# Kernel optimization log

Measured on AMD Instinct MI355X. Metric: run time of the kernel, lower is better.

## Reference

```python
import jax, jax.numpy as jnp
from jax import lax
import numpy as np

BN_EPS = 1e-5
LEAKY_SLOPE = 0.1


def _conv(x, w, stride=1):
    # x: [B,Cin,H,W], w: [Cout,Cin,kh,kw], 'same' padding (padding = k//2)
    p = w.shape[2] // 2
    return lax.conv_general_dilated(x, w, (stride, stride), [(p, p), (p, p)],
                                    dimension_numbers=('NCHW', 'OIHW', 'NCHW'))


def _bn(x, g, b, m, v):
    scale = g / jnp.sqrt(v + BN_EPS)
    return x * scale[None, :, None, None] + (b - m * scale)[None, :, None, None]


def _leaky(x):
    return jnp.where(x >= 0, x, LEAKY_SLOPE * x)


def _identity_grid(s, dtype=jnp.float32):
    # F.affine_grid identity, align_corners=True: grid[i,j] = (x_j, y_i), coords in [-1,1]
    xs = jnp.linspace(-1.0, 1.0, s, dtype=dtype)
    gx, gy = jnp.meshgrid(xs, xs)  # gx[i,j]=xs[j], gy[i,j]=xs[i]
    return jnp.stack([gx, gy], axis=-1)[None]  # [1,s,s,2]


def _grid_sample(img, grid):
    # torch.nn.functional.grid_sample, bilinear, align_corners=True, padding_mode='zeros'
    # img: [B,C,H,W], grid: [B,h,w,2] with grid[...,0]=x(width), grid[...,1]=y(height)
    B, C, H, W = img.shape
    x = (grid[..., 0] + 1.0) * 0.5 * (W - 1)
    y = (grid[..., 1] + 1.0) * 0.5 * (H - 1)
    x0f = jnp.floor(x)
    y0f = jnp.floor(y)
    x0 = x0f.astype(jnp.int32)
    y0 = y0f.astype(jnp.int32)
    x1 = x0 + 1
    y1 = y0 + 1
    wx1 = x - x0f
    wx0 = 1.0 - wx1
    wy1 = y - y0f
    wy0 = 1.0 - wy1

    def corner(xi, yi, w):
        m = ((xi >= 0) & (xi < W) & (yi >= 0) & (yi < H)).astype(img.dtype)
        xc = jnp.clip(xi, 0, W - 1)
        yc = jnp.clip(yi, 0, H - 1)
        gath = jax.vmap(lambda im, yy, xx: im[:, yy, xx])(img, yc, xc)  # [B,C,h,w]
        return gath * (w * m)[:, None]

    return (corner(x0, y0, wx0 * wy0) + corner(x1, y0, wx1 * wy0) +
            corner(x0, y1, wx0 * wy1) + corner(x1, y1, wx1 * wy1))


def _correlation(tgt_list, src_list):
    # corr[b, t, h, w] = sum_c tgt[b,c,t] * src[b,c,(h,w)], concat over feature layers (dim 1)
    outs = []
    for t, s in zip(tgt_list, src_list):
        B, C, H, W = t.shape
        c = jnp.einsum('bct,bcs->bts', t.reshape(B, C, H * W), s.reshape(B, C, H * W))
        outs.append(c.reshape(B, H * W, H, W))
    return jnp.concatenate(outs, axis=1)


def _stn_block(corr, i, w0, bn0_g, bn0_b, bn0_m, bn0_v, w1, bn1_g, bn1_b, bn1_m, bn1_v,
               w2, bn2_g, bn2_b, bn2_m, bn2_v, w3, b3):
    # downscale_factor == 1 (output_size == input_size), upsample-to-same-size is identity
    x = _leaky(_bn(_conv(corr, w0[i], stride=1), bn0_g[i], bn0_b[i], bn0_m[i], bn0_v[i]))
    x = _leaky(_bn(_conv(x, w1[i]), bn1_g[i], bn1_b[i], bn1_m[i], bn1_v[i]))
    x = _leaky(_bn(_conv(x, w2[i]), bn2_g[i], bn2_b[i], bn2_m[i], bn2_v[i]))
    x = _conv(x, w3[i]) + b3[i][None, :, None, None]
    return x  # [B,2,S,S]


def setup_inputs() -> dict:
    key = jax.random.key(0)
    ks = iter(jax.random.split(key, 16))
    B, C, S, L, NS = 8, 256, 32, 2, 3  # batch, feat channels, spatial, n feature layers, n scales
    HW = S * S
    d = {
        'src_layer2': jax.random.normal(next(ks), (B, C, S, S), jnp.float32) * 0.1,
        'src_layer3': jax.random.normal(next(ks), (B, C, S, S), jnp.float32) * 0.1,
        'tgt_layer2': jax.random.normal(next(ks), (B, C, S, S), jnp.float32) * 0.1,
        'tgt_layer3': jax.random.normal(next(ks), (B, C, S, S), jnp.float32) * 0.1,
        'w0': jax.random.normal(next(ks), (NS, HW, HW * L, 1, 1), jnp.float32) * 0.02,
        'w1': jax.random.normal(next(ks), (NS, HW // 2, HW, 3, 3), jnp.float32) * 0.02,
        'w2': jax.random.normal(next(ks), (NS, HW // 4, HW // 2, 3, 3), jnp.float32) * 0.02,
        'w3': jax.random.normal(next(ks), (NS, 2, HW // 4, 1, 1), jnp.float32) * 0.02,
        'b3': jnp.zeros((NS, 2), jnp.float32),
    }
    for j, ch in [(0, HW), (1, HW // 2), (2, HW // 4)]:
        d[f'bn{j}_g'] = jnp.ones((NS, ch), jnp.float32)
        d[f'bn{j}_b'] = jnp.zeros((NS, ch), jnp.float32)
        d[f'bn{j}_m'] = jnp.zeros((NS, ch), jnp.float32)
        d[f'bn{j}_v'] = jnp.ones((NS, ch), jnp.float32)
    return d


def reference(src_layer2, src_layer3, tgt_layer2, tgt_layer3,
              w0, bn0_g, bn0_b, bn0_m, bn0_v,
              w1, bn1_g, bn1_b, bn1_m, bn1_v,
              w2, bn2_g, bn2_b, bn2_m, bn2_v,
              w3, b3):
    src = [src_layer2, src_layer3]
    tgt = [tgt_layer2, tgt_layer3]
    S = src_layer2.shape[-1]
    ident = _identity_grid(S, src_layer2.dtype)  # [1,S,S,2]
    params = (w0, bn0_g, bn0_b, bn0_m, bn0_v, w1, bn1_g, bn1_b, bn1_m, bn1_v,
              w2, bn2_g, bn2_b, bn2_m, bn2_v, w3, b3)

    corr = _correlation(tgt, src)
    flow = jnp.transpose(_stn_block(corr, 0, *params), (0, 2, 3, 1)) + ident  # [B,S,S,2]
    n_scales = w0.shape[0]
    for i in range(1, n_scales):
        warped = [_grid_sample(s, flow) for s in src]
        corr = _correlation(tgt, warped)
        flow = flow + jnp.transpose(_stn_block(corr, i, *params), (0, 2, 3, 1))
    return flow
```

## Files before the change

### kernel.cpp

```cpp
#include <hip/hip_runtime.h>
#include <cstdint>
#include <cstddef>


typedef unsigned short u16;
using bf16x8 = __attribute__((ext_vector_type(8))) short;
using f32x4  = __attribute__((ext_vector_type(4))) float;

constexpr float BN_EPS = 1e-5f;
constexpr float SLOPE  = 0.1f;

__device__ __forceinline__ u16 f2bf(float f) {
    union { float f; uint32_t u; } c; c.f = f;
    uint32_t u = c.u;
    return (u16)((u + 0x7fffu + ((u >> 16) & 1u)) >> 16);
}
__device__ __forceinline__ float bf2f(u16 h) {
    union { uint32_t u; float f; } c; c.u = ((uint32_t)h) << 16;
    return c.f;
}

#define MFMA16(a, b, c) __builtin_amdgcn_mfma_f32_16x16x32_bf16(a, b, c, 0, 0, 0)

constexpr size_t OFF_TGT2B  = 0;
constexpr size_t OFF_TGT3B  = 2097152;
constexpr size_t OFF_SRCT2  = 4194304;
constexpr size_t OFF_SRCT3  = 6291456;
constexpr size_t OFF_WARPT2 = 8388608;
constexpr size_t OFF_WARPT3 = 10485760;
constexpr size_t OFF_W0B    = 12582912;
constexpr size_t OFF_WPK1   = 14680064;
constexpr size_t OFF_WPK2   = 19398656;
constexpr size_t OFF_E      = 20578304;
constexpr size_t OFF_X0T    = 24772608;
constexpr size_t OFF_FLOW   = 33161216;

__global__ __launch_bounds__(256) void cvt_kernel(
    const float* __restrict__ in, u16* __restrict__ out, int n)
{
    int i = (blockIdx.x * 256 + threadIdx.x) * 4;
    if (i + 3 < n) {
        float4 v = *(const float4*)(in + i);
        ushort4 o;
        o.x = f2bf(v.x); o.y = f2bf(v.y); o.z = f2bf(v.z); o.w = f2bf(v.w);
        *(ushort4*)(out + i) = o;
    }
}

__global__ __launch_bounds__(256) void transpose_cvt(
    const float* __restrict__ in, u16* __restrict__ out)
{
    __shared__ float tile[32][33];
    const int s0 = blockIdx.x * 32;
    const int c0 = blockIdx.y * 32;
    const int b  = blockIdx.z;
    const int tid = threadIdx.x;
    const int tx = tid & 31, ty = tid >> 5;
    const float* ib = in + ((size_t)b * 256 + c0) * 1024 + s0;
    #pragma unroll
    for (int r = 0; r < 4; ++r)
        tile[ty + r * 8][tx] = ib[(size_t)(ty + r * 8) * 1024 + tx];
    __syncthreads();
    u16* ob = out + ((size_t)b * 1024 + s0) * 256 + c0;
    #pragma unroll
    for (int r = 0; r < 4; ++r) {
        int s = ty + r * 8;
        ob[(size_t)s * 256 + tx] = f2bf(tile[tx][s]);
    }
}

__global__ __launch_bounds__(256) void pack_conv_w(
    const float* __restrict__ w, u16* __restrict__ out, int COUT, int CIN)
{
    int idx = blockIdx.x * 256 + threadIdx.x;
    if (idx >= COUT * CIN) return;
    int o = idx / CIN, c = idx - o * CIN;
    const float* g = w + (size_t)idx * 9;
    u16* ob = out + (size_t)o * 9 * CIN + c;
    #pragma unroll
    for (int t = 0; t < 9; ++t) ob[(size_t)t * CIN] = f2bf(g[t]);
}

__global__ __launch_bounds__(256) void e_gemm(
    const u16* __restrict__ w0b,
    const u16* __restrict__ tgt2b,
    const u16* __restrict__ tgt3b,
    u16* __restrict__ E)
{
    __shared__ u16 ash[128 * 64];
    __shared__ u16 bsh[128 * 64];
    const int c0 = blockIdx.x * 128;
    const int o0 = blockIdx.y * 128;
    const int b  = blockIdx.z >> 1;
    const int l  = blockIdx.z & 1;
    const u16* tgt = (l == 0 ? tgt2b : tgt3b) + (size_t)b * 262144;
    const int tid = threadIdx.x, lane = tid & 63, wid = tid >> 6;
    const int wm = (wid >> 1) * 64, wn = (wid & 1) * 64;

    f32x4 acc[4][4];
    #pragma unroll
    for (int i = 0; i < 4; ++i)
        #pragma unroll
        for (int j = 0; j < 4; ++j) acc[i][j] = (f32x4){0.f, 0.f, 0.f, 0.f};

    for (int k0 = 0; k0 < 1024; k0 += 64) {
        #pragma unroll
        for (int p = 0; p < 4; ++p) {
            int idx = p * 256 + tid;
            int row = idx >> 3, s = idx & 7;
            *(bf16x8*)&ash[row * 64 + ((s ^ (row & 7)) << 3)] =
                *(const bf16x8*)(w0b + (size_t)(o0 + row) * 2048 + l * 1024 + k0 + s * 8);
            *(bf16x8*)&bsh[row * 64 + ((s ^ (row & 7)) << 3)] =
                *(const bf16x8*)(tgt + (size_t)(c0 + row) * 1024 + k0 + s * 8);
        }
        __syncthreads();
        #pragma unroll
        for (int kk = 0; kk < 2; ++kk) {
            bf16x8 af[4], bfr[4];
            #pragma unroll
            for (int i = 0; i < 4; ++i) {
                int row = wm + i * 16 + (lane & 15);
                int s = kk * 4 + (lane >> 4);
                af[i] = *(const bf16x8*)&ash[row * 64 + ((s ^ (row & 7)) << 3)];
                int rowb = wn + i * 16 + (lane & 15);
                bfr[i] = *(const bf16x8*)&bsh[rowb * 64 + ((s ^ (rowb & 7)) << 3)];
            }
            #pragma unroll
            for (int i = 0; i < 4; ++i)
                #pragma unroll
                for (int j = 0; j < 4; ++j)
                    acc[i][j] = MFMA16(af[i], bfr[j], acc[i][j]);
        }
        __syncthreads();
    }
    u16* Eb = E + ((size_t)blockIdx.z * 1024 + o0) * 256 + c0;
    #pragma unroll
    for (int i = 0; i < 4; ++i)
        #pragma unroll
        for (int j = 0; j < 4; ++j)
            #pragma unroll
            for (int r = 0; r < 4; ++r) {
                int m = wm + i * 16 + ((lane >> 4) << 2) + r;
                int n = wn + j * 16 + (lane & 15);
                Eb[(size_t)m * 256 + n] = f2bf(acc[i][j][r]);
            }
}

__global__ __launch_bounds__(256) void x0_gemm(
    const u16* __restrict__ sA2,
    const u16* __restrict__ sA3,
    const u16* __restrict__ E,
    const float* __restrict__ bng, const float* __restrict__ bnb,
    const float* __restrict__ bnm, const float* __restrict__ bnv,
    u16* __restrict__ x0T)
{
    __shared__ u16 ash[128 * 64];
    __shared__ u16 bsh[128 * 64];
    const int o0 = blockIdx.x * 128;
    const int s0 = blockIdx.y * 128;
    const int b  = blockIdx.z;
    const int tid = threadIdx.x, lane = tid & 63, wid = tid >> 6;
    const int wm = (wid >> 1) * 64, wn = (wid & 1) * 64;

    f32x4 acc[4][4];
    #pragma unroll
    for (int i = 0; i < 4; ++i)
        #pragma unroll
        for (int j = 0; j < 4; ++j) acc[i][j] = (f32x4){0.f, 0.f, 0.f, 0.f};

    for (int kc = 0; kc < 8; ++kc) {
        const int l = kc >> 2;
        const int c0k = (kc & 3) * 64;
        const u16* sa = (l == 0 ? sA2 : sA3) + (size_t)b * 262144;
        const u16* eb = E + (size_t)((b << 1) + l) * 262144;
        #pragma unroll
        for (int p = 0; p < 4; ++p) {
            int idx = p * 256 + tid;
            int row = idx >> 3, s = idx & 7;
            *(bf16x8*)&ash[row * 64 + ((s ^ (row & 7)) << 3)] =
                *(const bf16x8*)(sa + (size_t)(s0 + row) * 256 + c0k + s * 8);
            *(bf16x8*)&bsh[row * 64 + ((s ^ (row & 7)) << 3)] =
                *(const bf16x8*)(eb + (size_t)(o0 + row) * 256 + c0k + s * 8);
        }
        __syncthreads();
        #pragma unroll
        for (int kk = 0; kk < 2; ++kk) {
            bf16x8 af[4], bfr[4];
            #pragma unroll
            for (int i = 0; i < 4; ++i) {
                int row = wm + i * 16 + (lane & 15);
                int s = kk * 4 + (lane >> 4);
                af[i] = *(const bf16x8*)&ash[row * 64 + ((s ^ (row & 7)) << 3)];
                int rowb = wn + i * 16 + (lane & 15);
                bfr[i] = *(const bf16x8*)&bsh[rowb * 64 + ((s ^ (rowb & 7)) << 3)];
            }
            #pragma unroll
            for (int i = 0; i < 4; ++i)
                #pragma unroll
                for (int j = 0; j < 4; ++j)
                    acc[i][j] = MFMA16(af[i], bfr[j], acc[i][j]);
        }
        __syncthreads();
    }
    #pragma unroll
    for (int j = 0; j < 4; ++j) {
        const int o = o0 + wn + j * 16 + (lane & 15);
        const float scv = bng[o] * rsqrtf(bnv[o] + BN_EPS);
        const float shv = bnb[o] - bnm[o] * scv;
        #pragma unroll
        for (int i = 0; i < 4; ++i)
            #pragma unroll
            for (int r = 0; r < 4; ++r) {
                int m = s0 + wm + i * 16 + ((lane >> 4) << 2) + r;
                float t = acc[i][j][r] * scv + shv;
                t = t >= 0.f ? t : SLOPE * t;
                x0T[((size_t)(b << 10) + m) * 1024 + o] = f2bf(t);
            }
    }
}

template<int CIN, int COUT>
__global__ __launch_bounds__(256) void conv_gemm(
    const u16* __restrict__ xin,
    const u16* __restrict__ wpk,
    const float* __restrict__ bng, const float* __restrict__ bnb,
    const float* __restrict__ bnm, const float* __restrict__ bnv,
    u16* __restrict__ xout)
{
    __shared__ u16 ash[9 * 64 * 32];
    __shared__ u16 bsh[340 * 56];
    const int o0 = blockIdx.x * 64;
    const int y0 = blockIdx.y * 8;
    const int b  = blockIdx.z;
    const int tid = threadIdx.x, lane = tid & 63, wid = tid >> 6;
    const int wn = wid * 64;
    const u16* xb = xin + (size_t)b * 1024 * CIN;

    f32x4 acc[4][4];
    #pragma unroll
    for (int i = 0; i < 4; ++i)
        #pragma unroll
        for (int j = 0; j < 4; ++j) acc[i][j] = (f32x4){0.f, 0.f, 0.f, 0.f};

    for (int c0 = 0; c0 < CIN; c0 += 32) {
        #pragma unroll
        for (int p = 0; p < 9; ++p) {
            int idx = p * 256 + tid;
            int t = idx >> 8, row = (idx >> 2) & 63, s = idx & 3;
            *(bf16x8*)&ash[(t * 64 + row) * 32 + ((s ^ (row & 3)) << 3)] =
                *(const bf16x8*)(wpk + ((size_t)(o0 + row) * 9 + t) * CIN + c0 + s * 8);
        }
        for (int idx = tid; idx < 1360; idx += 256) {
            int pos = idx >> 2, s = idx & 3;
            int py = pos / 34, px = pos - py * 34;
            int gy = y0 + py - 1, gx = px - 1;
            bf16x8 v = {0, 0, 0, 0, 0, 0, 0, 0};
            if (gy >= 0 && gy < 32 && gx >= 0 && gx < 32)
                v = *(const bf16x8*)&xb[(size_t)(gy * 32 + gx) * CIN + c0 + s * 8];
            *(bf16x8*)&bsh[pos * 56 + s * 8] = v;
        }
        __syncthreads();
        #pragma unroll
        for (int t = 0; t < 9; ++t) {
            const int dy = t / 3, dx = t - dy * 3;
            bf16x8 af[4], bfr[4];
            #pragma unroll
            for (int i = 0; i < 4; ++i) {
                int row = i * 16 + (lane & 15);
                int s = lane >> 4;
                af[i] = *(const bf16x8*)&ash[(t * 64 + row) * 32 + ((s ^ (row & 3)) << 3)];
            }
            #pragma unroll
            for (int j = 0; j < 4; ++j) {
                int n = wn + j * 16 + (lane & 15);
                int pos = ((n >> 5) + dy) * 34 + (n & 31) + dx;
                bfr[j] = *(const bf16x8*)&bsh[pos * 56 + ((lane >> 4) << 3)];
            }
            #pragma unroll
            for (int i = 0; i < 4; ++i)
                #pragma unroll
                for (int j = 0; j < 4; ++j)
                    acc[i][j] = MFMA16(af[i], bfr[j], acc[i][j]);
        }
        __syncthreads();
    }
    #pragma unroll
    for (int i = 0; i < 4; ++i) {
        float scv[4], shv[4];
        #pragma unroll
        for (int r = 0; r < 4; ++r) {
            int o = o0 + i * 16 + ((lane >> 4) << 2) + r;
            float s = bng[o] * rsqrtf(bnv[o] + BN_EPS);
            scv[r] = s; shv[r] = bnb[o] - bnm[o] * s;
        }
        #pragma unroll
        for (int j = 0; j < 4; ++j) {
            int n = wn + j * 16 + (lane & 15);
            int sg = y0 * 32 + n;
            ushort4 pk;
            float t0 = acc[i][j][0] * scv[0] + shv[0]; t0 = t0 >= 0.f ? t0 : SLOPE * t0;
            float t1 = acc[i][j][1] * scv[1] + shv[1]; t1 = t1 >= 0.f ? t1 : SLOPE * t1;
            float t2 = acc[i][j][2] * scv[2] + shv[2]; t2 = t2 >= 0.f ? t2 : SLOPE * t2;
            float t3 = acc[i][j][3] * scv[3] + shv[3]; t3 = t3 >= 0.f ? t3 : SLOPE * t3;
            pk.x = f2bf(t0); pk.y = f2bf(t1); pk.z = f2bf(t2); pk.w = f2bf(t3);
            *(ushort4*)&xout[((size_t)(b * 1024 + sg)) * COUT + o0 + i * 16 + ((lane >> 4) << 2)] = pk;
        }
    }
}

__global__ __launch_bounds__(64) void warp_kernel(
    const u16* __restrict__ srcT,
    const float* __restrict__ flow,
    u16* __restrict__ outT)
{
    const int bs = blockIdx.x;
    const int b = bs >> 10;
    const float fx = flow[(size_t)bs * 2 + 0];
    const float fy = flow[(size_t)bs * 2 + 1];
    const float px = (fx + 1.f) * 15.5f;
    const float py = (fy + 1.f) * 15.5f;
    const float x0f = floorf(px), y0f = floorf(py);
    const int x0 = (int)x0f, y0 = (int)y0f;
    const float wx1 = px - x0f, wx0 = 1.f - wx1;
    const float wy1 = py - y0f, wy0 = 1.f - wy1;
    const int lane = threadIdx.x;
    const u16* sb = srcT + (size_t)b * 262144 + lane * 4;
    float a0 = 0.f, a1 = 0.f, a2 = 0.f, a3 = 0.f;
    #pragma unroll
    for (int cr = 0; cr < 4; ++cr) {
        const int xi = x0 + (cr & 1), yi = y0 + (cr >> 1);
        const float w = (cr == 0 ? wx0 * wy0 : cr == 1 ? wx1 * wy0 :
                         cr == 2 ? wx0 * wy1 : wx1 * wy1);
        if (xi >= 0 && xi < 32 && yi >= 0 && yi < 32) {
            const ushort4 v = *(const ushort4*)(sb + (size_t)(yi * 32 + xi) * 256);
            a0 += w * bf2f(v.x); a1 += w * bf2f(v.y);
            a2 += w * bf2f(v.z); a3 += w * bf2f(v.w);
        }
    }
    ushort4 o;
    o.x = f2bf(a0); o.y = f2bf(a1); o.z = f2bf(a2); o.w = f2bf(a3);
    *(ushort4*)(outT + (size_t)bs * 256 + lane * 4) = o;
}

__global__ __launch_bounds__(256) void conv3_flow(
    const u16* __restrict__ x2T,
    const float* __restrict__ w3s,
    const float* __restrict__ b3s,
    float* __restrict__ flow, int add_ident)
{
    const int widx = blockIdx.x * 4 + (threadIdx.x >> 6);
    const int lane = threadIdx.x & 63;
    const ushort4 v = *(const ushort4*)&x2T[(size_t)widx * 256 + lane * 4];
    float a0 = 0.f, a1 = 0.f;
    const u16* vp = (const u16*)&v;
    #pragma unroll
    for (int j = 0; j < 4; ++j) {
        const float xv = bf2f(vp[j]);
        a0 += xv * w3s[lane * 4 + j];
        a1 += xv * w3s[256 + lane * 4 + j];
    }
    #pragma unroll
    for (int off = 32; off > 0; off >>= 1) {
        a0 += __shfl_down(a0, off);
        a1 += __shfl_down(a1, off);
    }
    if (lane == 0) {
        a0 += b3s[0]; a1 += b3s[1];
        float* f = flow + (size_t)widx * 2;
        if (add_ident) {
            const int s = widx & 1023;
            const int yy = s >> 5, xx = s & 31;
            f[0] = a0 + (-1.f + xx * (2.f / 31.f));
            f[1] = a1 + (-1.f + yy * (2.f / 31.f));
        } else {
            f[0] += a0;
            f[1] += a1;
        }
    }
}

__global__ __launch_bounds__(256) void copy_flow_kernel(
    const float* __restrict__ flow, float* __restrict__ out, int n)
{
    const int i = blockIdx.x * 256 + threadIdx.x;
    if (i < n) out[i] = flow[i];
}

extern "C" void kernel_launch(void* const* d_in, const int* in_sizes, int n_in,
                              void* d_out, int out_size, void* d_ws, size_t ws_size,
                              hipStream_t stream) {
    (void)in_sizes; (void)n_in; (void)ws_size;
    const float* src2 = (const float*)d_in[0];
    const float* src3 = (const float*)d_in[1];
    const float* tgt2 = (const float*)d_in[2];
    const float* tgt3 = (const float*)d_in[3];
    const float* w0   = (const float*)d_in[4];
    const float* w1   = (const float*)d_in[5];
    const float* w2   = (const float*)d_in[6];
    const float* w3   = (const float*)d_in[7];
    const float* b3   = (const float*)d_in[8];
    const float* bn0g = (const float*)d_in[9];
    const float* bn0b = (const float*)d_in[10];
    const float* bn0m = (const float*)d_in[11];
    const float* bn0v = (const float*)d_in[12];
    const float* bn1g = (const float*)d_in[13];
    const float* bn1b = (const float*)d_in[14];
    const float* bn1m = (const float*)d_in[15];
    const float* bn1v = (const float*)d_in[16];
    const float* bn2g = (const float*)d_in[17];
    const float* bn2b = (const float*)d_in[18];
    const float* bn2m = (const float*)d_in[19];
    const float* bn2v = (const float*)d_in[20];

    u16* ws = (u16*)d_ws;
    u16* tgt2b  = ws + OFF_TGT2B;
    u16* tgt3b  = ws + OFF_TGT3B;
    u16* srcT2  = ws + OFF_SRCT2;
    u16* srcT3  = ws + OFF_SRCT3;
    u16* warpT2 = ws + OFF_WARPT2;
    u16* warpT3 = ws + OFF_WARPT3;
    u16* w0b    = ws + OFF_W0B;
    u16* wpk1   = ws + OFF_WPK1;
    u16* wpk2   = ws + OFF_WPK2;
    u16* E      = ws + OFF_E;
    u16* x0T    = ws + OFF_X0T;
    u16* x1T    = ws + OFF_E;
    u16* x2T    = ws + OFF_WARPT2;
    float* flow = (float*)(ws + OFF_FLOW);

    cvt_kernel<<<2048, 256, 0, stream>>>(tgt2, tgt2b, 2097152);
    cvt_kernel<<<2048, 256, 0, stream>>>(tgt3, tgt3b, 2097152);
    transpose_cvt<<<dim3(32, 8, 8), 256, 0, stream>>>(src2, srcT2);
    transpose_cvt<<<dim3(32, 8, 8), 256, 0, stream>>>(src3, srcT3);

    for (int sc = 0; sc < 3; ++sc) {
        cvt_kernel<<<2048, 256, 0, stream>>>(w0 + (size_t)sc * 2097152, w0b, 2097152);
        pack_conv_w<<<2048, 256, 0, stream>>>(w1 + (size_t)sc * 4718592, wpk1, 512, 1024);
        pack_conv_w<<<512, 256, 0, stream>>>(w2 + (size_t)sc * 1179648, wpk2, 256, 512);

        const u16* a2 = srcT2;
        const u16* a3 = srcT3;
        if (sc > 0) {
            warp_kernel<<<8192, 64, 0, stream>>>(srcT2, flow, warpT2);
            warp_kernel<<<8192, 64, 0, stream>>>(srcT3, flow, warpT3);
            a2 = warpT2; a3 = warpT3;
        }
        e_gemm<<<dim3(2, 8, 16), 256, 0, stream>>>(w0b, tgt2b, tgt3b, E);
        x0_gemm<<<dim3(8, 8, 8), 256, 0, stream>>>(a2, a3, E,
            bn0g + sc * 1024, bn0b + sc * 1024, bn0m + sc * 1024, bn0v + sc * 1024, x0T);
        conv_gemm<1024, 512><<<dim3(8, 4, 8), 256, 0, stream>>>(x0T, wpk1,
            bn1g + sc * 512, bn1b + sc * 512, bn1m + sc * 512, bn1v + sc * 512, x1T);
        conv_gemm<512, 256><<<dim3(4, 4, 8), 256, 0, stream>>>(x1T, wpk2,
            bn2g + sc * 256, bn2b + sc * 256, bn2m + sc * 256, bn2v + sc * 256, x2T);
        conv3_flow<<<2048, 256, 0, stream>>>(x2T, w3 + sc * 512, b3 + sc * 2,
                                             flow, sc == 0 ? 1 : 0);
    }
    copy_flow_kernel<<<64, 256, 0, stream>>>(flow, (float*)d_out, out_size);
}
```

Before: 906.4 us.

## Use zero-padded activation layout and smaller spatial tiles in conv GEMMs

Stores the x0 and x1 activations in a 34x34 spatially padded layout, with pad rows and columns zeroed by a new kernel. The conv halo load becomes an unconditional contiguous copy with no bounds checks. The conv kernels are templated on rows per block (4 and 2 instead of 8), which multiplies the block count to fill more compute units, and the LDS stride and swizzle are changed. The cost is extra zeroing launches and more redundant halo and weight loads per output.

```diff
diff --git a/kernel.cpp b/kernel.cpp
--- a/kernel.cpp
+++ b/kernel.cpp
@@ -28,12 +28,11 @@
 constexpr size_t OFF_SRCT3  = 6291456;
 constexpr size_t OFF_WARPT2 = 8388608;
 constexpr size_t OFF_WARPT3 = 10485760;
-constexpr size_t OFF_W0B    = 12582912;
-constexpr size_t OFF_WPK1   = 14680064;
-constexpr size_t OFF_WPK2   = 19398656;
-constexpr size_t OFF_E      = 20578304;
-constexpr size_t OFF_X0T    = 24772608;
-constexpr size_t OFF_FLOW   = 33161216;
+constexpr size_t OFF_WPK1   = 12582912;
+constexpr size_t OFF_WPK2   = 17301504;
+constexpr size_t OFF_EX1    = 18481152;
+constexpr size_t OFF_X0P    = 23216128;
+constexpr size_t OFF_FLOW   = 32686080;
 
 __global__ __launch_bounds__(256) void cvt_kernel(
     const float* __restrict__ in, u16* __restrict__ out, int n)
@@ -79,6 +78,22 @@
     u16* ob = out + (size_t)o * 9 * CIN + c;
     #pragma unroll
     for (int t = 0; t < 9; ++t) ob[(size_t)t * CIN] = f2bf(g[t]);
+}
+
+template<int C>
+__global__ __launch_bounds__(256) void zero_pads(u16* __restrict__ xP)
+{
+    constexpr int NC = C / 8;
+    int idx = blockIdx.x * 256 + threadIdx.x;
+    if (idx >= 8 * 132 * NC) return;
+    int c8  = idx & (NC - 1);
+    int rem = idx / NC;
+    int b = rem / 132, j = rem - b * 132;
+    int pos;
+    if (j < 34)      pos = j;
+    else if (j < 68) pos = 1122 + (j - 34);
+    else { int k = j - 68; pos = ((k >> 1) + 1) * 34 + (k & 1) * 33; }
+    *(bf16x8*)&xP[((size_t)b * 1156 + pos) * C + c8 * 8] = (bf16x8){0,0,0,0,0,0,0,0};
 }
 
 __global__ __launch_bounds__(256) void e_gemm(
@@ -152,7 +167,7 @@
     const u16* __restrict__ E,
     const float* __restrict__ bng, const float* __restrict__ bnb,
     const float* __restrict__ bnm, const float* __restrict__ bnv,
-    u16* __restrict__ x0T)
+    u16* __restrict__ x0P)
 {
     __shared__ u16 ash[128 * 64];
     __shared__ u16 bsh[128 * 64];
@@ -214,72 +229,71 @@
                 int m = s0 + wm + i * 16 + ((lane >> 4) << 2) + r;
                 float t = acc[i][j][r] * scv + shv;
                 t = t >= 0.f ? t : SLOPE * t;
-                x0T[((size_t)(b << 10) + m) * 1024 + o] = f2bf(t);
-            }
-    }
-}
-
-template<int CIN, int COUT>
+                size_t sp = (size_t)b * 1156 + ((m >> 5) + 1) * 34 + (m & 31) + 1;
+                x0P[sp * 1024 + o] = f2bf(t);
+            }
+    }
+}
+
+template<int CIN, int COUT, int NT, bool PADOUT>
 __global__ __launch_bounds__(256) void conv_gemm(
-    const u16* __restrict__ xin,
+    const u16* __restrict__ xinP,
     const u16* __restrict__ wpk,
     const float* __restrict__ bng, const float* __restrict__ bnb,
     const float* __restrict__ bnm, const float* __restrict__ bnv,
     u16* __restrict__ xout)
 {
+    constexpr int NPOS = (NT + 2) * 34;
+    constexpr int JT = NT / 2;
     __shared__ u16 ash[9 * 64 * 32];
-    __shared__ u16 bsh[340 * 56];
+    __shared__ u16 bsh[NPOS * 36];
     const int o0 = blockIdx.x * 64;
-    const int y0 = blockIdx.y * 8;
+    const int y0 = blockIdx.y * NT;
     const int b  = blockIdx.z;
     const int tid = threadIdx.x, lane = tid & 63, wid = tid >> 6;
-    const int wn = wid * 64;
-    const u16* xb = xin + (size_t)b * 1024 * CIN;
-
-    f32x4 acc[4][4];
+    const int wn = wid * (NT * 8);
+    const u16* xpb = xinP + ((size_t)b * 1156 + y0 * 34) * CIN;
+
+    f32x4 acc[4][JT];
     #pragma unroll
     for (int i = 0; i < 4; ++i)
         #pragma unroll
-        for (int j = 0; j < 4; ++j) acc[i][j] = (f32x4){0.f, 0.f, 0.f, 0.f};
+        for (int j = 0; j < JT; ++j) acc[i][j] = (f32x4){0.f, 0.f, 0.f, 0.f};
 
     for (int c0 = 0; c0 < CIN; c0 += 32) {
         #pragma unroll
         for (int p = 0; p < 9; ++p) {
             int idx = p * 256 + tid;
-            int t = idx >> 8, row = (idx >> 2) & 63, s = idx & 3;
-            *(bf16x8*)&ash[(t * 64 + row) * 32 + ((s ^ (row & 3)) << 3)] =
-                *(const bf16x8*)(wpk + ((size_t)(o0 + row) * 9 + t) * CIN + c0 + s * 8);
-        }
-        for (int idx = tid; idx < 1360; idx += 256) {
+            int row = (idx >> 2) & 63, s = idx & 3;
+            *(bf16x8*)&ash[((p * 64 + row) << 5) + ((s ^ ((row >> 1) & 3)) << 3)] =
+                *(const bf16x8*)(wpk + ((size_t)(o0 + row) * 9 + p) * CIN + c0 + s * 8);
+        }
+        for (int idx = tid; idx < NPOS * 4; idx += 256) {
             int pos = idx >> 2, s = idx & 3;
-            int py = pos / 34, px = pos - py * 34;
-            int gy = y0 + py - 1, gx = px - 1;
-            bf16x8 v = {0, 0, 0, 0, 0, 0, 0, 0};
-            if (gy >= 0 && gy < 32 && gx >= 0 && gx < 32)
-                v = *(const bf16x8*)&xb[(size_t)(gy * 32 + gx) * CIN + c0 + s * 8];
-            *(bf16x8*)&bsh[pos * 56 + s * 8] = v;
+            *(bf16x8*)&bsh[pos * 36 + s * 8] =
+                *(const bf16x8*)(xpb + (size_t)pos * CIN + c0 + s * 8);
         }
         __syncthreads();
         #pragma unroll
         for (int t = 0; t < 9; ++t) {
             const int dy = t / 3, dx = t - dy * 3;
-            bf16x8 af[4], bfr[4];
+            bf16x8 af[4], bfr[JT];
             #pragma unroll
             for (int i = 0; i < 4; ++i) {
                 int row = i * 16 + (lane & 15);
-                int s = lane >> 4;
-                af[i] = *(const bf16x8*)&ash[(t * 64 + row) * 32 + ((s ^ (row & 3)) << 3)];
-            }
-            #pragma unroll
-            for (int j = 0; j < 4; ++j) {
+                af[i] = *(const bf16x8*)&ash[((t * 64 + row) << 5) +
+                                             (((lane >> 4) ^ ((row >> 1) & 3)) << 3)];
+            }
+            #pragma unroll
+            for (int j = 0; j < JT; ++j) {
                 int n = wn + j * 16 + (lane & 15);
                 int pos = ((n >> 5) + dy) * 34 + (n & 31) + dx;
-                bfr[j] = *(const bf16x8*)&bsh[pos * 56 + ((lane >> 4) << 3)];
+                bfr[j] = *(const bf16x8*)&bsh[pos * 36 + ((lane >> 4) << 3)];
             }
             #pragma unroll
             for (int i = 0; i < 4; ++i)
                 #pragma unroll
-                for (int j = 0; j < 4; ++j)
+                for (int j = 0; j < JT; ++j)
                     acc[i][j] = MFMA16(af[i], bfr[j], acc[i][j]);
         }
         __syncthreads();
@@ -294,16 +308,18 @@
             scv[r] = s; shv[r] = bnb[o] - bnm[o] * s;
         }
         #pragma unroll
-        for (int j = 0; j < 4; ++j) {
+        for (int j = 0; j < JT; ++j) {
             int n = wn + j * 16 + (lane & 15);
-            int sg = y0 * 32 + n;
+            int yg = y0 + (n >> 5), xg = n & 31;
+            size_t sp = PADOUT ? ((size_t)b * 1156 + (size_t)(yg + 1) * 34 + xg + 1)
+                               : ((size_t)b * 1024 + (size_t)yg * 32 + xg);
             ushort4 pk;
             float t0 = acc[i][j][0] * scv[0] + shv[0]; t0 = t0 >= 0.f ? t0 : SLOPE * t0;
             float t1 = acc[i][j][1] * scv[1] + shv[1]; t1 = t1 >= 0.f ? t1 : SLOPE * t1;
             float t2 = acc[i][j][2] * scv[2] + shv[2]; t2 = t2 >= 0.f ? t2 : SLOPE * t2;
             float t3 = acc[i][j][3] * scv[3] + shv[3]; t3 = t3 >= 0.f ? t3 : SLOPE * t3;
             pk.x = f2bf(t0); pk.y = f2bf(t1); pk.z = f2bf(t2); pk.w = f2bf(t3);
-            *(ushort4*)&xout[((size_t)(b * 1024 + sg)) * COUT + o0 + i * 16 + ((lane >> 4) << 2)] = pk;
+            *(ushort4*)&xout[sp * COUT + o0 + i * 16 + ((lane >> 4) << 2)] = pk;
         }
     }
 }
@@ -419,12 +435,12 @@
     u16* srcT3  = ws + OFF_SRCT3;
     u16* warpT2 = ws + OFF_WARPT2;
     u16* warpT3 = ws + OFF_WARPT3;
-    u16* w0b    = ws + OFF_W0B;
     u16* wpk1   = ws + OFF_WPK1;
     u16* wpk2   = ws + OFF_WPK2;
-    u16* E      = ws + OFF_E;
-    u16* x0T    = ws + OFF_X0T;
-    u16* x1T    = ws + OFF_E;
+    u16* E      = ws + OFF_EX1;
+    u16* x1P    = ws + OFF_EX1;
+    u16* x0P    = ws + OFF_X0P;
+    u16* w0b    = ws + OFF_X0P;
     u16* x2T    = ws + OFF_WARPT2;
     float* flow = (float*)(ws + OFF_FLOW);
 
@@ -446,11 +462,13 @@
             a2 = warpT2; a3 = warpT3;
         }
         e_gemm<<<dim3(2, 8, 16), 256, 0, stream>>>(w0b, tgt2b, tgt3b, E);
+        zero_pads<1024><<<528, 256, 0, stream>>>(x0P);
         x0_gemm<<<dim3(8, 8, 8), 256, 0, stream>>>(a2, a3, E,
-            bn0g + sc * 1024, bn0b + sc * 1024, bn0m + sc * 1024, bn0v + sc * 1024, x0T);
-        conv_gemm<1024, 512><<<dim3(8, 4, 8), 256, 0, stream>>>(x0T, wpk1,
-            bn1g + sc * 512, bn1b + sc * 512, bn1m + sc * 512, bn1v + sc * 512, x1T);
-        conv_gemm<512, 256><<<dim3(4, 4, 8), 256, 0, stream>>>(x1T, wpk2,
+            bn0g + sc * 1024, bn0b + sc * 1024, bn0m + sc * 1024, bn0v + sc * 1024, x0P);
+        zero_pads<512><<<264, 256, 0, stream>>>(x1P);
+        conv_gemm<1024, 512, 4, true><<<dim3(8, 8, 8), 256, 0, stream>>>(x0P, wpk1,
+            bn1g + sc * 512, bn1b + sc * 512, bn1m + sc * 512, bn1v + sc * 512, x1P);
+        conv_gemm<512, 256, 2, false><<<dim3(4, 16, 8), 256, 0, stream>>>(x1P, wpk2,
             bn2g + sc * 256, bn2b + sc * 256, bn2m + sc * 256, bn2v + sc * 256, x2T);
         conv3_flow<<<2048, 256, 0, stream>>>(x2T, w3 + sc * 512, b3 + sc * 2,
                                              flow, sc == 0 ? 1 : 0);
```

Result: faster. 806.4 us (-11.0%).
